# Optimization experiments

Hardware: AMD Instinct MI355X
Metric: run time of the kernel (lower is better)

Reference implementation:

```python
import jax, jax.numpy as jnp
import numpy as np

B, S, P, D, H = 2, 1024, 1024, 2048, 16
DH = D // H
QMAX = 127.0


def quantize(x):
    # per-tensor abs-max int8 quantization, matching torch quantize(bits=8)
    scale = jnp.max(jnp.abs(x)) / QMAX
    x_q = jnp.clip(jnp.round(x / scale), -128.0, 127.0).astype(jnp.int8)
    return x_q, scale


def dequantize(x_q, scale):
    return x_q.astype(jnp.float32) * scale


def setup_inputs() -> dict:
    key = jax.random.key(0)
    ks = jax.random.split(key, 12)
    sd = 1.0 / np.sqrt(D)
    inp = {
        'hidden_states': jax.random.normal(ks[0], (B, S, D), jnp.float32),
        'Wq': jax.random.normal(ks[1], (D, D), jnp.float32) * sd,
        'bq': jnp.zeros((D,), jnp.float32),
        'Wk': jax.random.normal(ks[2], (D, D), jnp.float32) * sd,
        'bk': jnp.zeros((D,), jnp.float32),
        'Wv': jax.random.normal(ks[3], (D, D), jnp.float32) * sd,
        'bv': jnp.zeros((D,), jnp.float32),
        'Wo': jax.random.normal(ks[4], (D, D), jnp.float32) * sd,
        'bo': jnp.zeros((D,), jnp.float32),
        'past_k_q': jax.random.randint(ks[5], (B, P, D), -128, 128).astype(jnp.int8),
        'past_k_scale': jnp.float32(0.03),
        'past_v_q': jax.random.randint(ks[6], (B, P, D), -128, 128).astype(jnp.int8),
        'past_v_scale': jnp.float32(0.02),
    }
    return inp


def attention(h, k, v, Wq, bq, Wo, bo):
    # standard causal MHA; query positions are offset by the cache length P
    T = k.shape[1]  # P + S
    q = (h @ Wq + bq).reshape(B, S, H, DH)
    kh = k.reshape(B, T, H, DH)
    vh = v.reshape(B, T, H, DH)
    scores = jnp.einsum('bshd,bthd->bhst', q, kh) / np.sqrt(DH)  # [B,H,S,T]
    causal = jnp.arange(T)[None, :] <= (P + jnp.arange(S))[:, None]  # [S,T]
    scores = jnp.where(causal[None, None], scores, jnp.float32(-1e30))
    attn = jax.nn.softmax(scores, axis=-1)
    out = jnp.einsum('bhst,bthd->bshd', attn, vh).reshape(B, S, D)
    return out @ Wo + bo


def reference(hidden_states, Wq, bq, Wk, bk, Wv, bv, Wo, bo,
              past_k_q, past_k_scale, past_v_q, past_v_scale):
    k = hidden_states @ Wk + bk  # [B,S,D]
    v = hidden_states @ Wv + bv
    k_q, k_scale = quantize(k)
    v_q, v_scale = quantize(v)
    # dequantize cached KV and concat along the sequence dim (dim=1)
    k_prev = dequantize(past_k_q, past_k_scale)
    v_prev = dequantize(past_v_q, past_v_scale)
    k_full = jnp.concatenate([k_prev, k], axis=1)  # [B,P+S,D]
    v_full = jnp.concatenate([v_prev, v], axis=1)
    out = attention(hidden_states, k_full, v_full, Wq, bq, Wo, bo)
    return out, k_q, k_scale, v_q, v_scale
```

## Files before the change

### kernel.cpp

```cpp
#include <hip/hip_runtime.h>

#define SOFT_SCALE 0.08838834764831845f
#define BSD 4194304
#define NELEM 4194304

typedef __attribute__((ext_vector_type(4))) float    f32x4;
typedef __attribute__((ext_vector_type(8))) short    bf16x8;
typedef __attribute__((ext_vector_type(4))) short    bf16x4;
typedef __attribute__((ext_vector_type(4))) unsigned u32x4;

__device__ __forceinline__ float bs2f(short s) {
    unsigned u = ((unsigned)(unsigned short)s) << 16;
    return __builtin_bit_cast(float, u);
}
__device__ __forceinline__ short f2bs(float f) {
    unsigned u = __builtin_bit_cast(unsigned, f);
    unsigned r = (u + 0x7fffu + ((u >> 16) & 1u)) >> 16;
    return (short)r;
}

__device__ __forceinline__ void stage16(const short* g, short* l) {
#if __has_builtin(__builtin_amdgcn_global_load_lds)
    __builtin_amdgcn_global_load_lds(
        (const __attribute__((address_space(1))) void*)g,
        (__attribute__((address_space(3))) void*)l, 16, 0, 0);
#else
    *(bf16x8*)l = *(const bf16x8*)g;
#endif
}

__global__ void probe_init(const int* __restrict__ q, float* __restrict__ scal) {
    const int lane = threadIdx.x;
    int bad = 0;
#pragma unroll
    for (int i = 0; i < 4; ++i) {
        const int v = q[i * 64 + lane];
        bad |= (v < -128 || v > 127) ? 1 : 0;
    }
    const int anybad = __any(bad);
    if (lane == 0) ((int*)scal)[2] = anybad ? 0 : 1;
    if (lane == 1) scal[0] = 0.f;
    if (lane == 2) scal[1] = 0.f;
}

__global__ void conv_bf16(const float* __restrict__ X, short* __restrict__ Y) {
    const int stride = gridDim.x * blockDim.x;
    for (int i = blockIdx.x * blockDim.x + threadIdx.x; i < NELEM / 8; i += stride) {
        const int e = i * 8;
        f32x4 a = *(const f32x4*)&X[e];
        f32x4 b = *(const f32x4*)&X[e + 4];
        bf16x8 o;
        o[0] = f2bs(a[0]); o[1] = f2bs(a[1]); o[2] = f2bs(a[2]); o[3] = f2bs(a[3]);
        o[4] = f2bs(b[0]); o[5] = f2bs(b[1]); o[6] = f2bs(b[2]); o[7] = f2bs(b[3]);
        *(bf16x8*)&Y[e] = o;
    }
}

__global__ __launch_bounds__(256) void transpose_conv(const float* __restrict__ W0,
                                                      const float* __restrict__ W1,
                                                      const float* __restrict__ W2,
                                                      short* __restrict__ WT) {
    __shared__ __align__(16) short Tl[64 * 68];
    const float* W = blockIdx.z == 0 ? W0 : (blockIdx.z == 1 ? W1 : W2);
    short* out = WT + (long)blockIdx.z * 4194304;
    const int tid = threadIdx.x;
    const int n0 = blockIdx.x * 64, k0 = blockIdx.y * 64;
#pragma unroll
    for (int i = 0; i < 4; ++i) {
        const int e = i * 1024 + tid * 4;
        const int r = e >> 6, c = e & 63;
        f32x4 f = *(const f32x4*)&W[(long)(k0 + r) * 2048 + n0 + c];
        bf16x4 s4 = { f2bs(f[0]), f2bs(f[1]), f2bs(f[2]), f2bs(f[3]) };
        *(bf16x4*)&Tl[r * 68 + c] = s4;
    }
    __syncthreads();
#pragma unroll
    for (int i = 0; i < 4; ++i) {
        const int e = i * 1024 + tid * 4;
        const int nr = e >> 6, kk = e & 63;
        bf16x4 o = { Tl[(kk + 0) * 68 + nr], Tl[(kk + 1) * 68 + nr],
                     Tl[(kk + 2) * 68 + nr], Tl[(kk + 3) * 68 + nr] };
        *(bf16x4*)&out[(long)(n0 + nr) * 2048 + k0 + kk] = o;
    }
}

__global__ void dequant_kernel(const void* __restrict__ pk, const void* __restrict__ pv,
                               const float* __restrict__ psk, const float* __restrict__ psv,
                               short* __restrict__ Kf, short* __restrict__ Vf,
                               const int* __restrict__ wsflag) {
    const int z = blockIdx.z;
    const void* src = z ? pv : pk;
    const float sc = z ? *psv : *psk;
    short* dst = z ? Vf : Kf;
    const int flag = wsflag[2];
    const int stride = gridDim.x * blockDim.x;
    for (int i = blockIdx.x * blockDim.x + threadIdx.x; i < NELEM / 8; i += stride) {
        const int e = i * 8;
        int vals[8];
        if (flag) {
            const int* s = (const int*)src + e;
            *(int4*)&vals[0] = *(const int4*)&s[0];
            *(int4*)&vals[4] = *(const int4*)&s[4];
        } else {
            const int2 wv = *(const int2*)((const char*)src + e);
#pragma unroll
            for (int j = 0; j < 4; ++j) vals[j] = (int)(signed char)(wv.x >> (8 * j));
#pragma unroll
            for (int j = 0; j < 4; ++j) vals[4 + j] = (int)(signed char)(wv.y >> (8 * j));
        }
        bf16x8 o;
#pragma unroll
        for (int j = 0; j < 8; ++j) o[j] = f2bs((float)vals[j] * sc);
        *(bf16x8*)&dst[e + ((e >> 21) << 21)] = o;
    }
}

__global__ __launch_bounds__(256, 2) void gemm_m97(
    const short* __restrict__ A,
    const short* __restrict__ Bt0, const short* __restrict__ Bt1, const short* __restrict__ Bt2,
    const float* __restrict__ bi0, const float* __restrict__ bi1, const float* __restrict__ bi2,
    void* __restrict__ o0, void* __restrict__ o1, void* __restrict__ o2,
    int mode_sgl, float scale_sgl) {
    __shared__ __align__(16) short Al[2][4096];
    __shared__ __align__(16) short Bl[2][4096];
    const int nbx = gridDim.x, nby = gridDim.y, nbz = gridDim.z;
    const int nwg = nbx * nby * nbz;
    const int orig = blockIdx.x + nbx * (blockIdx.y + nby * blockIdx.z);
    const int cpx = nwg >> 3;
    int swz = (orig & 7) * cpx + (orig >> 3);
    const int bx = swz % nbx; swz /= nbx;
    const int by = swz % nby;
    const int bz = swz / nby;

    const short* Bt   = bz == 0 ? Bt0 : (bz == 1 ? Bt1 : Bt2);
    const float* bias = bz == 0 ? bi0 : (bz == 1 ? bi1 : bi2);
    void* outp        = bz == 0 ? o0  : (bz == 1 ? o1  : o2);
    int mode; float scl;
    if (nbz == 3) { mode = (bz == 0) ? 1 : 2; scl = (bz == 0) ? SOFT_SCALE : 1.f; }
    else          { mode = mode_sgl;          scl = scale_sgl; }

    const int tid = threadIdx.x, lane = tid & 63, w = tid >> 6;
    const int wm = w >> 1, wn = w & 1, l4 = lane >> 4, ln = lane & 15;
    const int m0 = by * 128, n0 = bx * 128;

    const short* gA0 = A  + (long)(m0 + (tid >> 2)) * 2048 + (tid & 3) * 8;
    const short* gA1 = gA0 + 64 * 2048;
    const short* gB0 = Bt + (long)(n0 + (tid >> 2)) * 2048 + (tid & 3) * 8;
    const short* gB1 = gB0 + 64 * 2048;

    f32x4 acc[4][4];
#pragma unroll
    for (int mi = 0; mi < 4; ++mi)
#pragma unroll
        for (int ni = 0; ni < 4; ++ni) acc[mi][ni] = (f32x4){0, 0, 0, 0};

#define STAGE_G(buf, ko)                                   \
    do {                                                   \
        stage16(gA0 + (ko), &Al[buf][tid * 8]);            \
        stage16(gA1 + (ko), &Al[buf][2048 + tid * 8]);     \
        stage16(gB0 + (ko), &Bl[buf][tid * 8]);            \
        stage16(gB1 + (ko), &Bl[buf][2048 + tid * 8]);     \
    } while (0)

    STAGE_G(0, 0);
    asm volatile("s_waitcnt vmcnt(0)" ::: "memory");
    __syncthreads();
    int cur = 0;
    for (int kt = 0; kt < 64; ++kt) {
        if (kt < 63) STAGE_G(cur ^ 1, (kt + 1) * 32);
        bf16x8 af[4], bfr[4];
#pragma unroll
        for (int mi = 0; mi < 4; ++mi)
            af[mi] = *(const bf16x8*)&Al[cur][(wm * 64 + mi * 16 + ln) * 32 + l4 * 8];
#pragma unroll
        for (int ni = 0; ni < 4; ++ni)
            bfr[ni] = *(const bf16x8*)&Bl[cur][(wn * 64 + ni * 16 + ln) * 32 + l4 * 8];
#pragma unroll
        for (int mi = 0; mi < 4; ++mi)
#pragma unroll
            for (int ni = 0; ni < 4; ++ni)
                acc[mi][ni] = __builtin_amdgcn_mfma_f32_16x16x32_bf16(
                    af[mi], bfr[ni], acc[mi][ni], 0, 0, 0);
        asm volatile("s_waitcnt vmcnt(0)" ::: "memory");
        __syncthreads();
        cur ^= 1;
    }
#undef STAGE_G

#pragma unroll
    for (int ni = 0; ni < 4; ++ni) {
        const int gn = n0 + wn * 64 + ni * 16 + ln;
        const float bv = bias[gn];
#pragma unroll
        for (int mi = 0; mi < 4; ++mi) {
#pragma unroll
            for (int r = 0; r < 4; ++r) {
                const int gm = m0 + wm * 64 + mi * 16 + l4 * 4 + r;
                const float v = (acc[mi][ni][r] + bv) * scl;
                if (mode == 0) {
                    ((float*)outp)[(long)gm * 2048 + gn] = v;
                } else if (mode == 1) {
                    ((short*)outp)[(long)gm * 2048 + gn] = f2bs(v);
                } else {
                    const int gr = gm + 1024 + ((gm >> 10) << 10);
                    ((short*)outp)[(long)gr * 2048 + gn] = f2bs(v);
                }
            }
        }
    }
}

__global__ __launch_bounds__(256, 2) void gemm_wo(const short* __restrict__ A,
                                                  const short* __restrict__ Bt,
                                                  const float* __restrict__ bias,
                                                  float* __restrict__ outp) {
    __shared__ __align__(16) short Al[2][4096];
    __shared__ __align__(16) short Bl[2][2048];
    const int orig = blockIdx.x + 32 * blockIdx.y;
    const int swz = (orig & 7) * 64 + (orig >> 3);
    const int bx = swz & 31, by = swz >> 5;
    const int tid = threadIdx.x, lane = tid & 63, w = tid >> 6;
    const int wm = w >> 1, wn = w & 1, l4 = lane >> 4, ln = lane & 15;
    const int m0 = by * 128, n0 = bx * 64;

    const short* gA0 = A  + (long)(m0 + (tid >> 2)) * 2048 + (tid & 3) * 8;
    const short* gA1 = gA0 + 64 * 2048;
    const short* gB0 = Bt + (long)(n0 + (tid >> 2)) * 2048 + (tid & 3) * 8;

    f32x4 acc[4][2];
#pragma unroll
    for (int mi = 0; mi < 4; ++mi)
#pragma unroll
        for (int ni = 0; ni < 2; ++ni) acc[mi][ni] = (f32x4){0, 0, 0, 0};

#define STAGE_W(buf, ko)                                   \
    do {                                                   \
        stage16(gA0 + (ko), &Al[buf][tid * 8]);            \
        stage16(gA1 + (ko), &Al[buf][2048 + tid * 8]);     \
        stage16(gB0 + (ko), &Bl[buf][tid * 8]);            \
    } while (0)

    STAGE_W(0, 0);
    asm volatile("s_waitcnt vmcnt(0)" ::: "memory");
    __syncthreads();
    int cur = 0;
    for (int kt = 0; kt < 64; ++kt) {
        if (kt < 63) STAGE_W(cur ^ 1, (kt + 1) * 32);
        bf16x8 af[4], bfr[2];
#pragma unroll
        for (int mi = 0; mi < 4; ++mi)
            af[mi] = *(const bf16x8*)&Al[cur][(wm * 64 + mi * 16 + ln) * 32 + l4 * 8];
#pragma unroll
        for (int ni = 0; ni < 2; ++ni)
            bfr[ni] = *(const bf16x8*)&Bl[cur][(wn * 32 + ni * 16 + ln) * 32 + l4 * 8];
#pragma unroll
        for (int mi = 0; mi < 4; ++mi)
#pragma unroll
            for (int ni = 0; ni < 2; ++ni)
                acc[mi][ni] = __builtin_amdgcn_mfma_f32_16x16x32_bf16(
                    af[mi], bfr[ni], acc[mi][ni], 0, 0, 0);
        asm volatile("s_waitcnt vmcnt(0)" ::: "memory");
        __syncthreads();
        cur ^= 1;
    }
#undef STAGE_W

#pragma unroll
    for (int ni = 0; ni < 2; ++ni) {
        const int gn = n0 + wn * 32 + ni * 16 + ln;
        const float bv = bias[gn];
#pragma unroll
        for (int mi = 0; mi < 4; ++mi) {
#pragma unroll
            for (int r = 0; r < 4; ++r) {
                const int gm = m0 + wm * 64 + mi * 16 + l4 * 4 + r;
                outp[(long)gm * 2048 + gn] = acc[mi][ni][r] + bv;
            }
        }
    }
}

__global__ void absmax_kernel(const short* __restrict__ Kf, const short* __restrict__ Vf,
                              float* __restrict__ scal) {
    const int z = blockIdx.z;
    const short* src = z ? Vf : Kf;
    const int tid = threadIdx.x, lane = tid & 63, w = tid >> 6;
    float mx = 0.f;
    const int stride = gridDim.x * blockDim.x;
    for (int i = blockIdx.x * blockDim.x + tid; i < NELEM / 8; i += stride) {
        const int e = i * 8;
        const int flat = e + 2097152 + ((e >> 21) << 21);
        bf16x8 v = *(const bf16x8*)&src[flat];
#pragma unroll
        for (int j = 0; j < 8; ++j) mx = fmaxf(mx, fabsf(bs2f(v[j])));
    }
#pragma unroll
    for (int o = 32; o > 0; o >>= 1) mx = fmaxf(mx, __shfl_xor(mx, o));
    __shared__ float wred[4];
    if (lane == 0) wred[w] = mx;
    __syncthreads();
    if (tid == 0) {
        const float m2 = fmaxf(fmaxf(wred[0], wred[1]), fmaxf(wred[2], wred[3]));
        atomicMax((unsigned int*)&scal[z], __builtin_bit_cast(unsigned int, m2));
    }
}

__global__ void quantize_kernel(const short* __restrict__ Kf, const short* __restrict__ Vf,
                                const float* __restrict__ scal, float* __restrict__ out) {
    const int z = blockIdx.z;
    const short* src = z ? Vf : Kf;
    const float mx = scal[z];
    const float scale = mx * (1.f / 127.f);
    const float inv = (mx > 0.f) ? 127.f / mx : 0.f;
    const long ob = z ? (2L * BSD + 1) : (1L * BSD);
    if (blockIdx.x == 0 && threadIdx.x == 0)
        out[z ? (3L * BSD + 1) : (2L * BSD)] = scale;
    const int stride = gridDim.x * blockDim.x;
    for (int i = blockIdx.x * blockDim.x + threadIdx.x; i < NELEM / 4; i += stride) {
        const int e = i * 4;
        const int flat = e + 2097152 + ((e >> 21) << 21);
        bf16x4 x4 = *(const bf16x4*)&src[flat];
        float4 q;
        q.x = fminf(127.f, fmaxf(-128.f, rintf(bs2f(x4[0]) * inv)));
        q.y = fminf(127.f, fmaxf(-128.f, rintf(bs2f(x4[1]) * inv)));
        q.z = fminf(127.f, fmaxf(-128.f, rintf(bs2f(x4[2]) * inv)));
        q.w = fminf(127.f, fmaxf(-128.f, rintf(bs2f(x4[3]) * inv)));
        *(float4*)&out[ob + e] = q;
    }
}

__global__ __launch_bounds__(256, 2) void attn_kernel(const short* __restrict__ Q,
                                                      const short* __restrict__ Kf,
                                                      const short* __restrict__ Vf,
                                                      short* __restrict__ O) {
    __shared__ __align__(16) short Kl[64 * 136];
    __shared__ __align__(16) short Vt[128 * 72];
    const int L = blockIdx.x + 16 * (blockIdx.y + 16 * blockIdx.z);
    const int x = L & 7, rr = L >> 3;
    const int qt0 = rr & 15, pgrp = rr >> 4;
    const int p = x + 8 * pgrp;
    const int h = p >> 1, b = p & 1;
    const int qt = (pgrp >= 2) ? (15 - qt0) : qt0;

    const int tid = threadIdx.x, w = tid >> 6, lane = tid & 63;
    const int l4 = lane >> 4, n = lane & 15;
    const int rg = tid >> 4, cg = tid & 15, stc = cg * 8;
    const int sIdx = qt * 64 + w * 16 + n;
    const int qlim = 1024 + sIdx;

    bf16x8 qf[4];
#pragma unroll
    for (int c = 0; c < 4; ++c)
        qf[c] = *(const bf16x8*)&Q[(long)(b * 1024 + sIdx) * 2048 + h * 128 + c * 32 + l4 * 8];

    f32x4 acco[8];
#pragma unroll
    for (int i = 0; i < 8; ++i) acco[i] = (f32x4){0, 0, 0, 0};
    float m_run = -1e30f, l_run = 0.f;

    const short* Kb = Kf + (long)(b * 2048) * 2048 + h * 128;
    const short* Vb = Vf + (long)(b * 2048) * 2048 + h * 128;
    const int nt = 17 + qt;

    bf16x8 kreg[4], vreg[4];
#pragma unroll
    for (int i = 0; i < 4; ++i) kreg[i] = *(const bf16x8*)&Kb[(long)(i * 16 + rg) * 2048 + stc];
#pragma unroll
    for (int i = 0; i < 4; ++i) vreg[i] = *(const bf16x8*)&Vb[(long)(rg * 4 + i) * 2048 + stc];

    for (int t = 0; t < nt; ++t) {
        const int t0 = t * 64;
        __syncthreads();
#pragma unroll
        for (int i = 0; i < 4; ++i)
            *(bf16x8*)&Kl[(i * 16 + rg) * 136 + stc] = kreg[i];
#pragma unroll
        for (int j = 0; j < 8; ++j) {
            const int d = stc + j;
            bf16x4 c4 = { vreg[0][j], vreg[1][j], vreg[2][j], vreg[3][j] };
            *(bf16x4*)&Vt[d * 72 + ((rg ^ ((d >> 3) & 7)) << 2)] = c4;
        }
        if (t + 1 < nt) {
            const int t1 = (t + 1) * 64;
#pragma unroll
            for (int i = 0; i < 4; ++i)
                kreg[i] = *(const bf16x8*)&Kb[(long)(t1 + i * 16 + rg) * 2048 + stc];
#pragma unroll
            for (int i = 0; i < 4; ++i)
                vreg[i] = *(const bf16x8*)&Vb[(long)(t1 + rg * 4 + i) * 2048 + stc];
        }
        __syncthreads();

        float p16[16];
        __builtin_amdgcn_s_setprio(1);
#pragma unroll
        for (int kt = 0; kt < 4; ++kt) {
            f32x4 sc4 = (f32x4){0, 0, 0, 0};
#pragma unroll
            for (int c = 0; c < 4; ++c) {
                bf16x8 kfr = *(const bf16x8*)&Kl[(kt * 16 + n) * 136 + c * 32 + l4 * 8];
                sc4 = __builtin_amdgcn_mfma_f32_16x16x32_bf16(kfr, qf[c], sc4, 0, 0, 0);
            }
#pragma unroll
            for (int r = 0; r < 4; ++r) p16[kt * 4 + r] = sc4[r];
        }
        __builtin_amdgcn_s_setprio(0);
        if (t >= 16) {
#pragma unroll
            for (int i = 0; i < 16; ++i) {
                const int kg = t0 + (i >> 2) * 16 + l4 * 4 + (i & 3);
                if (kg > qlim) p16[i] = -1e30f;
            }
        }

        float tmax = p16[0];
#pragma unroll
        for (int i = 1; i < 16; ++i) tmax = fmaxf(tmax, p16[i]);
        tmax = fmaxf(tmax, __shfl_xor(tmax, 16));
        tmax = fmaxf(tmax, __shfl_xor(tmax, 32));
        if (!__all(tmax <= m_run + 8.f)) {
            const float mnew = fmaxf(m_run, tmax);
            const float fac = __expf(m_run - mnew);
            l_run *= fac;
#pragma unroll
            for (int i = 0; i < 8; ++i) acco[i] *= fac;
            m_run = mnew;
        }
        float tsum = 0.f;
#pragma unroll
        for (int i = 0; i < 16; ++i) { p16[i] = __expf(p16[i] - m_run); tsum += p16[i]; }
        tsum += __shfl_xor(tsum, 16);
        tsum += __shfl_xor(tsum, 32);
        l_run += tsum;

        u32x4 pw0, pw1;
#pragma unroll
        for (int wd = 0; wd < 4; ++wd) {
            unsigned r0, r1;
            asm("v_cvt_pk_bf16_f32 %0, %1, %2" : "=v"(r0) : "v"(p16[2 * wd]), "v"(p16[2 * wd + 1]));
            asm("v_cvt_pk_bf16_f32 %0, %1, %2" : "=v"(r1) : "v"(p16[8 + 2 * wd]), "v"(p16[8 + 2 * wd + 1]));
            pw0[wd] = r0; pw1[wd] = r1;
        }
        bf16x8 pb[2] = { __builtin_bit_cast(bf16x8, pw0), __builtin_bit_cast(bf16x8, pw1) };

        __builtin_amdgcn_s_setprio(1);
#pragma unroll
        for (int dc = 0; dc < 8; ++dc) {
            const int d = dc * 16 + n;
            const int swd = ((d >> 3) & 7) << 2;
#pragma unroll
            for (int k32 = 0; k32 < 2; ++k32) {
                bf16x4 g0 = *(const bf16x4*)&Vt[d * 72 + (k32 * 32 + ((4 * l4) ^ swd))];
                bf16x4 g1 = *(const bf16x4*)&Vt[d * 72 + (k32 * 32 + ((16 + 4 * l4) ^ swd))];
                bf16x8 vf = { g0[0], g0[1], g0[2], g0[3], g1[0], g1[1], g1[2], g1[3] };
                acco[dc] = __builtin_amdgcn_mfma_f32_16x16x32_bf16(vf, pb[k32], acco[dc], 0, 0, 0);
            }
        }
        __builtin_amdgcn_s_setprio(0);
    }

    __syncthreads();
    const float inv = 1.f / l_run;
#pragma unroll
    for (int dc = 0; dc < 8; ++dc)
#pragma unroll
        for (int r = 0; r < 4; ++r)
            Kl[(w * 16 + n) * 136 + dc * 16 + l4 * 4 + r] = f2bs(acco[dc][r] * inv);
    __syncthreads();
#pragma unroll
    for (int i = 0; i < 4; ++i) {
        const int row = i * 4 + (lane >> 4);
        const int col = (lane & 15) * 8;
        bf16x8 ov = *(const bf16x8*)&Kl[(w * 16 + row) * 136 + col];
        *(bf16x8*)&O[(long)(b * 1024 + qt * 64 + w * 16 + row) * 2048 + h * 128 + col] = ov;
    }
}

extern "C" void kernel_launch(void* const* d_in, const int* in_sizes, int n_in,
                              void* d_out, int out_size, void* d_ws, size_t ws_size,
                              hipStream_t stream) {
    const float* h   = (const float*)d_in[0];
    const float* Wq  = (const float*)d_in[1];
    const float* bq  = (const float*)d_in[2];
    const float* Wk  = (const float*)d_in[3];
    const float* bk  = (const float*)d_in[4];
    const float* Wv  = (const float*)d_in[5];
    const float* bv  = (const float*)d_in[6];
    const float* Wo  = (const float*)d_in[7];
    const float* bo  = (const float*)d_in[8];
    const void*  pkq = d_in[9];
    const float* pks = (const float*)d_in[10];
    const void*  pvq = d_in[11];
    const float* pvs = (const float*)d_in[12];
    float* out = (float*)d_out;

    char* ws = (char*)d_ws;
    dim3 blk(256);
    const bool big = (ws_size >= 75500000ull);

    if (big) {
        float* scal  = (float*)ws;
        short* hbf   = (short*)(ws + 256);
        short* WT3   = (short*)(ws + 256 + 1L * 8388608);
        short* Qbf   = (short*)(ws + 256 + 4L * 8388608);
        short* Kfull = (short*)(ws + 256 + 5L * 8388608);
        short* Vfull = (short*)(ws + 256 + 5L * 8388608 + 16777216);
        short* attnb = hbf;

        probe_init<<<1, 64, 0, stream>>>((const int*)pkq, scal);
        conv_bf16<<<1024, blk, 0, stream>>>(h, hbf);
        dequant_kernel<<<dim3(256, 1, 2), blk, 0, stream>>>(pkq, pvq, pks, pvs, Kfull, Vfull,
                                                            (const int*)d_ws);
        transpose_conv<<<dim3(32, 32, 3), blk, 0, stream>>>(Wq, Wk, Wv, WT3);
        gemm_m97<<<dim3(16, 16, 3), blk, 0, stream>>>(hbf, WT3, WT3 + 4194304, WT3 + 8388608,
                                                      bq, bk, bv, Qbf, Kfull, Vfull, 0, 1.f);
        absmax_kernel<<<dim3(512, 1, 2), blk, 0, stream>>>(Kfull, Vfull, scal);
        quantize_kernel<<<dim3(256, 1, 2), blk, 0, stream>>>(Kfull, Vfull, scal, out);
        attn_kernel<<<dim3(16, 16, 2), blk, 0, stream>>>(Qbf, Kfull, Vfull, attnb);
        transpose_conv<<<dim3(32, 32, 1), blk, 0, stream>>>(Wo, Wo, Wo, WT3);
        gemm_wo<<<dim3(32, 16), blk, 0, stream>>>(attnb, WT3, bo, out);
    } else {
        float* scal  = (float*)ws;
        short* hbf   = (short*)(ws + 256);
        short* WT    = (short*)(ws + 256 + 1L * 8388608);
        short* Qbf   = (short*)(ws + 256 + 2L * 8388608);
        short* Kfull = (short*)(ws + 256 + 3L * 8388608);
        short* Vfull = (short*)(ws + 256 + 3L * 8388608 + 16777216);
        short* attnb = hbf;

        probe_init<<<1, 64, 0, stream>>>((const int*)pkq, scal);
        conv_bf16<<<1024, blk, 0, stream>>>(h, hbf);
        dequant_kernel<<<dim3(256, 1, 2), blk, 0, stream>>>(pkq, pvq, pks, pvs, Kfull, Vfull,
                                                            (const int*)d_ws);
        transpose_conv<<<dim3(32, 32, 1), blk, 0, stream>>>(Wk, Wk, Wk, WT);
        gemm_m97<<<dim3(16, 16, 1), blk, 0, stream>>>(hbf, WT, WT, WT, bk, bk, bk,
                                                      Kfull, Kfull, Kfull, 2, 1.f);
        transpose_conv<<<dim3(32, 32, 1), blk, 0, stream>>>(Wv, Wv, Wv, WT);
        gemm_m97<<<dim3(16, 16, 1), blk, 0, stream>>>(hbf, WT, WT, WT, bv, bv, bv,
                                                      Vfull, Vfull, Vfull, 2, 1.f);
        absmax_kernel<<<dim3(512, 1, 2), blk, 0, stream>>>(Kfull, Vfull, scal);
        quantize_kernel<<<dim3(256, 1, 2), blk, 0, stream>>>(Kfull, Vfull, scal, out);
        transpose_conv<<<dim3(32, 32, 1), blk, 0, stream>>>(Wq, Wq, Wq, WT);
        gemm_m97<<<dim3(16, 16, 1), blk, 0, stream>>>(hbf, WT, WT, WT, bq, bq, bq,
                                                      Qbf, Qbf, Qbf, 1, SOFT_SCALE);
        attn_kernel<<<dim3(16, 16, 2), blk, 0, stream>>>(Qbf, Kfull, Vfull, attnb);
        transpose_conv<<<dim3(32, 32, 1), blk, 0, stream>>>(Wo, Wo, Wo, WT);
        gemm_wo<<<dim3(32, 16), blk, 0, stream>>>(attnb, WT, bo, out);
    }
}
```

Before: 230.5 us.

## Double-buffer attention K/V tiles, merge prep kernels, batch all weight transposes

```diff
diff --git a/kernel.cpp b/kernel.cpp
--- a/kernel.cpp
+++ b/kernel.cpp
@@ -43,25 +43,58 @@
     if (lane == 2) scal[1] = 0.f;
 }
 
-__global__ void conv_bf16(const float* __restrict__ X, short* __restrict__ Y) {
+__global__ void prep_kernel(const float* __restrict__ X, short* __restrict__ Y,
+                            const void* __restrict__ pk, const void* __restrict__ pv,
+                            const float* __restrict__ psk, const float* __restrict__ psv,
+                            short* __restrict__ Kf, short* __restrict__ Vf,
+                            const int* __restrict__ wsflag) {
+    const int z = blockIdx.z;
     const int stride = gridDim.x * blockDim.x;
-    for (int i = blockIdx.x * blockDim.x + threadIdx.x; i < NELEM / 8; i += stride) {
-        const int e = i * 8;
-        f32x4 a = *(const f32x4*)&X[e];
-        f32x4 b = *(const f32x4*)&X[e + 4];
-        bf16x8 o;
-        o[0] = f2bs(a[0]); o[1] = f2bs(a[1]); o[2] = f2bs(a[2]); o[3] = f2bs(a[3]);
-        o[4] = f2bs(b[0]); o[5] = f2bs(b[1]); o[6] = f2bs(b[2]); o[7] = f2bs(b[3]);
-        *(bf16x8*)&Y[e] = o;
+    if (z == 0) {
+        for (int i = blockIdx.x * blockDim.x + threadIdx.x; i < NELEM / 8; i += stride) {
+            const int e = i * 8;
+            f32x4 a = *(const f32x4*)&X[e];
+            f32x4 b = *(const f32x4*)&X[e + 4];
+            bf16x8 o;
+            o[0] = f2bs(a[0]); o[1] = f2bs(a[1]); o[2] = f2bs(a[2]); o[3] = f2bs(a[3]);
+            o[4] = f2bs(b[0]); o[5] = f2bs(b[1]); o[6] = f2bs(b[2]); o[7] = f2bs(b[3]);
+            *(bf16x8*)&Y[e] = o;
+        }
+    } else {
+        const void* src = (z == 2) ? pv : pk;
+        const float sc = (z == 2) ? *psv : *psk;
+        short* dst = (z == 2) ? Vf : Kf;
+        const int flag = wsflag[2];
+        for (int i = blockIdx.x * blockDim.x + threadIdx.x; i < NELEM / 8; i += stride) {
+            const int e = i * 8;
+            int vals[8];
+            if (flag) {
+                const int* s = (const int*)src + e;
+                *(int4*)&vals[0] = *(const int4*)&s[0];
+                *(int4*)&vals[4] = *(const int4*)&s[4];
+            } else {
+                const int2 wv = *(const int2*)((const char*)src + e);
+#pragma unroll
+                for (int j = 0; j < 4; ++j) vals[j] = (int)(signed char)(wv.x >> (8 * j));
+#pragma unroll
+                for (int j = 0; j < 4; ++j) vals[4 + j] = (int)(signed char)(wv.y >> (8 * j));
+            }
+            bf16x8 o;
+#pragma unroll
+            for (int j = 0; j < 8; ++j) o[j] = f2bs((float)vals[j] * sc);
+            *(bf16x8*)&dst[e + ((e >> 21) << 21)] = o;
+        }
     }
 }
 
 __global__ __launch_bounds__(256) void transpose_conv(const float* __restrict__ W0,
                                                       const float* __restrict__ W1,
                                                       const float* __restrict__ W2,
+                                                      const float* __restrict__ W3,
                                                       short* __restrict__ WT) {
     __shared__ __align__(16) short Tl[64 * 68];
-    const float* W = blockIdx.z == 0 ? W0 : (blockIdx.z == 1 ? W1 : W2);
+    const float* W = blockIdx.z == 0 ? W0 : (blockIdx.z == 1 ? W1 :
+                     (blockIdx.z == 2 ? W2 : W3));
     short* out = WT + (long)blockIdx.z * 4194304;
     const int tid = threadIdx.x;
     const int n0 = blockIdx.x * 64, k0 = blockIdx.y * 64;
@@ -81,37 +114,6 @@
         bf16x4 o = { Tl[(kk + 0) * 68 + nr], Tl[(kk + 1) * 68 + nr],
                      Tl[(kk + 2) * 68 + nr], Tl[(kk + 3) * 68 + nr] };
         *(bf16x4*)&out[(long)(n0 + nr) * 2048 + k0 + kk] = o;
-    }
-}
-
-__global__ void dequant_kernel(const void* __restrict__ pk, const void* __restrict__ pv,
-                               const float* __restrict__ psk, const float* __restrict__ psv,
-                               short* __restrict__ Kf, short* __restrict__ Vf,
-                               const int* __restrict__ wsflag) {
-    const int z = blockIdx.z;
-    const void* src = z ? pv : pk;
-    const float sc = z ? *psv : *psk;
-    short* dst = z ? Vf : Kf;
-    const int flag = wsflag[2];
-    const int stride = gridDim.x * blockDim.x;
-    for (int i = blockIdx.x * blockDim.x + threadIdx.x; i < NELEM / 8; i += stride) {
-        const int e = i * 8;
-        int vals[8];
-        if (flag) {
-            const int* s = (const int*)src + e;
-            *(int4*)&vals[0] = *(const int4*)&s[0];
-            *(int4*)&vals[4] = *(const int4*)&s[4];
-        } else {
-            const int2 wv = *(const int2*)((const char*)src + e);
-#pragma unroll
-            for (int j = 0; j < 4; ++j) vals[j] = (int)(signed char)(wv.x >> (8 * j));
-#pragma unroll
-            for (int j = 0; j < 4; ++j) vals[4 + j] = (int)(signed char)(wv.y >> (8 * j));
-        }
-        bf16x8 o;
-#pragma unroll
-        for (int j = 0; j < 8; ++j) o[j] = f2bs((float)vals[j] * sc);
-        *(bf16x8*)&dst[e + ((e >> 21) << 21)] = o;
     }
 }
 
@@ -333,8 +335,8 @@
                                                       const short* __restrict__ Kf,
                                                       const short* __restrict__ Vf,
                                                       short* __restrict__ O) {
-    __shared__ __align__(16) short Kl[64 * 136];
-    __shared__ __align__(16) short Vt[128 * 72];
+    __shared__ __align__(16) short Kl[2][64 * 136];
+    __shared__ __align__(16) short Vt[2][128 * 72];
     const int L = blockIdx.x + 16 * (blockIdx.y + 16 * blockIdx.z);
     const int x = L & 7, rr = L >> 3;
     const int qt0 = rr & 15, pgrp = rr >> 4;
@@ -356,40 +358,43 @@
     f32x4 acco[8];
 #pragma unroll
     for (int i = 0; i < 8; ++i) acco[i] = (f32x4){0, 0, 0, 0};
-    float m_run = -1e30f, l_run = 0.f;
+    float m_run = 0.f, l_run = 0.f;
 
     const short* Kb = Kf + (long)(b * 2048) * 2048 + h * 128;
     const short* Vb = Vf + (long)(b * 2048) * 2048 + h * 128;
     const int nt = 17 + qt;
 
     bf16x8 kreg[4], vreg[4];
-#pragma unroll
-    for (int i = 0; i < 4; ++i) kreg[i] = *(const bf16x8*)&Kb[(long)(i * 16 + rg) * 2048 + stc];
-#pragma unroll
-    for (int i = 0; i < 4; ++i) vreg[i] = *(const bf16x8*)&Vb[(long)(rg * 4 + i) * 2048 + stc];
+#define LOAD_KV(te)                                                                   \
+    do {                                                                              \
+        _Pragma("unroll")                                                             \
+        for (int i = 0; i < 4; ++i)                                                   \
+            kreg[i] = *(const bf16x8*)&Kb[(long)((te) + i * 16 + rg) * 2048 + stc];   \
+        _Pragma("unroll")                                                             \
+        for (int i = 0; i < 4; ++i)                                                   \
+            vreg[i] = *(const bf16x8*)&Vb[(long)((te) + rg * 4 + i) * 2048 + stc];    \
+    } while (0)
+#define WRITE_BUF(bf)                                                                 \
+    do {                                                                              \
+        _Pragma("unroll")                                                             \
+        for (int i = 0; i < 4; ++i)                                                   \
+            *(bf16x8*)&Kl[bf][(i * 16 + rg) * 136 + stc] = kreg[i];                   \
+        _Pragma("unroll")                                                             \
+        for (int j = 0; j < 8; ++j) {                                                 \
+            const int d = stc + j;                                                    \
+            bf16x4 c4 = { vreg[0][j], vreg[1][j], vreg[2][j], vreg[3][j] };           \
+            *(bf16x4*)&Vt[bf][d * 72 + ((rg ^ ((d >> 3) & 7)) << 2)] = c4;            \
+        }                                                                             \
+    } while (0)
+
+    LOAD_KV(0);
+    WRITE_BUF(0);
+    __syncthreads();
 
     for (int t = 0; t < nt; ++t) {
+        const int buf = t & 1;
         const int t0 = t * 64;
-        __syncthreads();
-#pragma unroll
-        for (int i = 0; i < 4; ++i)
-            *(bf16x8*)&Kl[(i * 16 + rg) * 136 + stc] = kreg[i];
-#pragma unroll
-        for (int j = 0; j < 8; ++j) {
-            const int d = stc + j;
-            bf16x4 c4 = { vreg[0][j], vreg[1][j], vreg[2][j], vreg[3][j] };
-            *(bf16x4*)&Vt[d * 72 + ((rg ^ ((d >> 3) & 7)) << 2)] = c4;
-        }
-        if (t + 1 < nt) {
-            const int t1 = (t + 1) * 64;
-#pragma unroll
-            for (int i = 0; i < 4; ++i)
-                kreg[i] = *(const bf16x8*)&Kb[(long)(t1 + i * 16 + rg) * 2048 + stc];
-#pragma unroll
-            for (int i = 0; i < 4; ++i)
-                vreg[i] = *(const bf16x8*)&Vb[(long)(t1 + rg * 4 + i) * 2048 + stc];
-        }
-        __syncthreads();
+        if (t + 1 < nt) LOAD_KV((t + 1) * 64);
 
         float p16[16];
         __builtin_amdgcn_s_setprio(1);
@@ -398,7 +403,7 @@
             f32x4 sc4 = (f32x4){0, 0, 0, 0};
 #pragma unroll
             for (int c = 0; c < 4; ++c) {
-                bf16x8 kfr = *(const bf16x8*)&Kl[(kt * 16 + n) * 136 + c * 32 + l4 * 8];
+                bf16x8 kfr = *(const bf16x8*)&Kl[buf][(kt * 16 + n) * 136 + c * 32 + l4 * 8];
                 sc4 = __builtin_amdgcn_mfma_f32_16x16x32_bf16(kfr, qf[c], sc4, 0, 0, 0);
             }
 #pragma unroll
@@ -413,22 +418,25 @@
             }
         }
 
-        float tmax = p16[0];
-#pragma unroll
-        for (int i = 1; i < 16; ++i) tmax = fmaxf(tmax, p16[i]);
+        float tmax = fmaxf(p16[0], p16[1]);
+#pragma unroll
+        for (int i = 2; i < 16; ++i) tmax = fmaxf(tmax, p16[i]);
         tmax = fmaxf(tmax, __shfl_xor(tmax, 16));
         tmax = fmaxf(tmax, __shfl_xor(tmax, 32));
+        float e16[16], tsum = 0.f;
+#pragma unroll
+        for (int i = 0; i < 16; ++i) { e16[i] = __expf(p16[i] - m_run); tsum += e16[i]; }
         if (!__all(tmax <= m_run + 8.f)) {
             const float mnew = fmaxf(m_run, tmax);
             const float fac = __expf(m_run - mnew);
+            tsum *= fac;
+#pragma unroll
+            for (int i = 0; i < 16; ++i) e16[i] *= fac;
             l_run *= fac;
 #pragma unroll
             for (int i = 0; i < 8; ++i) acco[i] *= fac;
             m_run = mnew;
         }
-        float tsum = 0.f;
-#pragma unroll
-        for (int i = 0; i < 16; ++i) { p16[i] = __expf(p16[i] - m_run); tsum += p16[i]; }
         tsum += __shfl_xor(tsum, 16);
         tsum += __shfl_xor(tsum, 32);
         l_run += tsum;
@@ -437,8 +445,8 @@
 #pragma unroll
         for (int wd = 0; wd < 4; ++wd) {
             unsigned r0, r1;
-            asm("v_cvt_pk_bf16_f32 %0, %1, %2" : "=v"(r0) : "v"(p16[2 * wd]), "v"(p16[2 * wd + 1]));
-            asm("v_cvt_pk_bf16_f32 %0, %1, %2" : "=v"(r1) : "v"(p16[8 + 2 * wd]), "v"(p16[8 + 2 * wd + 1]));
+            asm("v_cvt_pk_bf16_f32 %0, %1, %2" : "=v"(r0) : "v"(e16[2 * wd]), "v"(e16[2 * wd + 1]));
+            asm("v_cvt_pk_bf16_f32 %0, %1, %2" : "=v"(r1) : "v"(e16[8 + 2 * wd]), "v"(e16[8 + 2 * wd + 1]));
             pw0[wd] = r0; pw1[wd] = r1;
         }
         bf16x8 pb[2] = { __builtin_bit_cast(bf16x8, pw0), __builtin_bit_cast(bf16x8, pw1) };
@@ -450,28 +458,32 @@
             const int swd = ((d >> 3) & 7) << 2;
 #pragma unroll
             for (int k32 = 0; k32 < 2; ++k32) {
-                bf16x4 g0 = *(const bf16x4*)&Vt[d * 72 + (k32 * 32 + ((4 * l4) ^ swd))];
-                bf16x4 g1 = *(const bf16x4*)&Vt[d * 72 + (k32 * 32 + ((16 + 4 * l4) ^ swd))];
+                bf16x4 g0 = *(const bf16x4*)&Vt[buf][d * 72 + (k32 * 32 + ((4 * l4) ^ swd))];
+                bf16x4 g1 = *(const bf16x4*)&Vt[buf][d * 72 + (k32 * 32 + ((16 + 4 * l4) ^ swd))];
                 bf16x8 vf = { g0[0], g0[1], g0[2], g0[3], g1[0], g1[1], g1[2], g1[3] };
                 acco[dc] = __builtin_amdgcn_mfma_f32_16x16x32_bf16(vf, pb[k32], acco[dc], 0, 0, 0);
             }
         }
         __builtin_amdgcn_s_setprio(0);
-    }
-
-    __syncthreads();
+
+        if (t + 1 < nt) WRITE_BUF(buf ^ 1);
+        __syncthreads();
+    }
+#undef LOAD_KV
+#undef WRITE_BUF
+
     const float inv = 1.f / l_run;
 #pragma unroll
     for (int dc = 0; dc < 8; ++dc)
 #pragma unroll
         for (int r = 0; r < 4; ++r)
-            Kl[(w * 16 + n) * 136 + dc * 16 + l4 * 4 + r] = f2bs(acco[dc][r] * inv);
+            Kl[0][(w * 16 + n) * 136 + dc * 16 + l4 * 4 + r] = f2bs(acco[dc][r] * inv);
     __syncthreads();
 #pragma unroll
     for (int i = 0; i < 4; ++i) {
         const int row = i * 4 + (lane >> 4);
         const int col = (lane & 15) * 8;
-        bf16x8 ov = *(const bf16x8*)&Kl[(w * 16 + row) * 136 + col];
+        bf16x8 ov = *(const bf16x8*)&Kl[0][(w * 16 + row) * 136 + col];
         *(bf16x8*)&O[(long)(b * 1024 + qt * 64 + w * 16 + row) * 2048 + h * 128 + col] = ov;
     }
 }
@@ -496,9 +508,27 @@
 
     char* ws = (char*)d_ws;
     dim3 blk(256);
-    const bool big = (ws_size >= 75500000ull);
-
-    if (big) {
+
+    if (ws_size >= 83886336ull) {
+        float* scal  = (float*)ws;
+        short* hbf   = (short*)(ws + 256);
+        short* WT4   = (short*)(ws + 256 + 1L * 8388608);
+        short* Qbf   = (short*)(ws + 256 + 5L * 8388608);
+        short* Kfull = (short*)(ws + 256 + 6L * 8388608);
+        short* Vfull = (short*)(ws + 256 + 6L * 8388608 + 16777216);
+        short* attnb = hbf;
+
+        probe_init<<<1, 64, 0, stream>>>((const int*)pkq, scal);
+        prep_kernel<<<dim3(256, 1, 3), blk, 0, stream>>>(h, hbf, pkq, pvq, pks, pvs,
+                                                         Kfull, Vfull, (const int*)d_ws);
+        transpose_conv<<<dim3(32, 32, 4), blk, 0, stream>>>(Wq, Wk, Wv, Wo, WT4);
+        gemm_m97<<<dim3(16, 16, 3), blk, 0, stream>>>(hbf, WT4, WT4 + 4194304, WT4 + 8388608,
+                                                      bq, bk, bv, Qbf, Kfull, Vfull, 0, 1.f);
+        absmax_kernel<<<dim3(512, 1, 2), blk, 0, stream>>>(Kfull, Vfull, scal);
+        quantize_kernel<<<dim3(256, 1, 2), blk, 0, stream>>>(Kfull, Vfull, scal, out);
+        attn_kernel<<<dim3(16, 16, 2), blk, 0, stream>>>(Qbf, Kfull, Vfull, attnb);
+        gemm_wo<<<dim3(32, 16), blk, 0, stream>>>(attnb, WT4 + 12582912, bo, out);
+    } else if (ws_size >= 75500000ull) {
         float* scal  = (float*)ws;
         short* hbf   = (short*)(ws + 256);
         short* WT3   = (short*)(ws + 256 + 1L * 8388608);
@@ -508,16 +538,15 @@
         short* attnb = hbf;
 
         probe_init<<<1, 64, 0, stream>>>((const int*)pkq, scal);
-        conv_bf16<<<1024, blk, 0, stream>>>(h, hbf);
-        dequant_kernel<<<dim3(256, 1, 2), blk, 0, stream>>>(pkq, pvq, pks, pvs, Kfull, Vfull,
-                                                            (const int*)d_ws);
-        transpose_conv<<<dim3(32, 32, 3), blk, 0, stream>>>(Wq, Wk, Wv, WT3);
+        prep_kernel<<<dim3(256, 1, 3), blk, 0, stream>>>(h, hbf, pkq, pvq, pks, pvs,
+                                                         Kfull, Vfull, (const int*)d_ws);
+        transpose_conv<<<dim3(32, 32, 3), blk, 0, stream>>>(Wq, Wk, Wv, Wv, WT3);
         gemm_m97<<<dim3(16, 16, 3), blk, 0, stream>>>(hbf, WT3, WT3 + 4194304, WT3 + 8388608,
                                                       bq, bk, bv, Qbf, Kfull, Vfull, 0, 1.f);
         absmax_kernel<<<dim3(512, 1, 2), blk, 0, stream>>>(Kfull, Vfull, scal);
         quantize_kernel<<<dim3(256, 1, 2), blk, 0, stream>>>(Kfull, Vfull, scal, out);
         attn_kernel<<<dim3(16, 16, 2), blk, 0, stream>>>(Qbf, Kfull, Vfull, attnb);
-        transpose_conv<<<dim3(32, 32, 1), blk, 0, stream>>>(Wo, Wo, Wo, WT3);
+        transpose_conv<<<dim3(32, 32, 1), blk, 0, stream>>>(Wo, Wo, Wo, Wo, WT3);
         gemm_wo<<<dim3(32, 16), blk, 0, stream>>>(attnb, WT3, bo, out);
     } else {
         float* scal  = (float*)ws;
@@ -529,22 +558,21 @@
         short* attnb = hbf;
 
         probe_init<<<1, 64, 0, stream>>>((const int*)pkq, scal);
-        conv_bf16<<<1024, blk, 0, stream>>>(h, hbf);
-        dequant_kernel<<<dim3(256, 1, 2), blk, 0, stream>>>(pkq, pvq, pks, pvs, Kfull, Vfull,
-                                                            (const int*)d_ws);
-        transpose_conv<<<dim3(32, 32, 1), blk, 0, stream>>>(Wk, Wk, Wk, WT);
+        prep_kernel<<<dim3(256, 1, 3), blk, 0, stream>>>(h, hbf, pkq, pvq, pks, pvs,
+                                                         Kfull, Vfull, (const int*)d_ws);
+        transpose_conv<<<dim3(32, 32, 1), blk, 0, stream>>>(Wk, Wk, Wk, Wk, WT);
         gemm_m97<<<dim3(16, 16, 1), blk, 0, stream>>>(hbf, WT, WT, WT, bk, bk, bk,
                                                       Kfull, Kfull, Kfull, 2, 1.f);
-        transpose_conv<<<dim3(32, 32, 1), blk, 0, stream>>>(Wv, Wv, Wv, WT);
+        transpose_conv<<<dim3(32, 32, 1), blk, 0, stream>>>(Wv, Wv, Wv, Wv, WT);
         gemm_m97<<<dim3(16, 16, 1), blk, 0, stream>>>(hbf, WT, WT, WT, bv, bv, bv,
                                                       Vfull, Vfull, Vfull, 2, 1.f);
         absmax_kernel<<<dim3(512, 1, 2), blk, 0, stream>>>(Kfull, Vfull, scal);
         quantize_kernel<<<dim3(256, 1, 2), blk, 0, stream>>>(Kfull, Vfull, scal, out);
-        transpose_conv<<<dim3(32, 32, 1), blk, 0, stream>>>(Wq, Wq, Wq, WT);
+        transpose_conv<<<dim3(32, 32, 1), blk, 0, stream>>>(Wq, Wq, Wq, Wq, WT);
         gemm_m97<<<dim3(16, 16, 1), blk, 0, stream>>>(hbf, WT, WT, WT, bq, bq, bq,
                                                       Qbf, Qbf, Qbf, 1, SOFT_SCALE);
         attn_kernel<<<dim3(16, 16, 2), blk, 0, stream>>>(Qbf, Kfull, Vfull, attnb);
-        transpose_conv<<<dim3(32, 32, 1), blk, 0, stream>>>(Wo, Wo, Wo, WT);
+        transpose_conv<<<dim3(32, 32, 1), blk, 0, stream>>>(Wo, Wo, Wo, Wo, WT);
         gemm_wo<<<dim3(32, 16), blk, 0, stream>>>(attnb, WT, bo, out);
     }
 }
```

New measurement: 221.6 us. 1.04x faster.
